# Performance work log

Hardware: AMD Instinct MI355X
Metric: run time of the kernel (lower is better)

The kernel has to match this reference:

```python
import jax, jax.numpy as jnp
import numpy as np

B = 256          # graphs per batch
NPG = 512        # nodes per data graph
NG = B * NPG     # 131072 data-graph nodes
EG = NG * 8      # 1048576 data-graph edges
NQPG = 16        # nodes per query graph
NQ = B * NQPG    # 4096 query nodes
EQ = NQ * 8      # 32768 query edges
IN, H, L, OUT = 64, 128, 2, 1


def setup_inputs() -> dict:
    key = jax.random.key(0)
    ks = jax.random.split(key, 24)
    # edges constrained within each graph (offset + local index)
    g_off = jnp.repeat(jnp.arange(B, dtype=jnp.int32) * NPG, EG // B)
    q_off = jnp.repeat(jnp.arange(B, dtype=jnp.int32) * NQPG, EQ // B)
    inp = {
        "X": jax.random.normal(ks[0], (NG, IN), jnp.float32),
        "X_q": jax.random.normal(ks[1], (NQ, IN), jnp.float32),
        "g_src": g_off + jax.random.randint(ks[2], (EG,), 0, NPG, jnp.int32),
        "g_dst": g_off + jax.random.randint(ks[3], (EG,), 0, NPG, jnp.int32),
        "g_n2g": jnp.repeat(jnp.arange(B, dtype=jnp.int32), NPG),
        "q_src": q_off + jax.random.randint(ks[4], (EQ,), 0, NQPG, jnp.int32),
        "q_dst": q_off + jax.random.randint(ks[5], (EQ,), 0, NQPG, jnp.int32),
        "q_n2g": jnp.repeat(jnp.arange(B, dtype=jnp.int32), NQPG),
    }
    def lin(k, fi, fo):
        s = 1.0 / np.sqrt(fi)
        return jax.random.uniform(k, (fi, fo), jnp.float32, -s, s)
    inp["Wg"] = lin(ks[6], IN, H); inp["bg"] = jnp.zeros((H,), jnp.float32)
    inp["Wq"] = lin(ks[7], IN, H); inp["bq"] = jnp.zeros((H,), jnp.float32)
    inp["betas_g"] = jnp.ones((L,), jnp.float32)  # AGNN beta, init 1
    inp["betas_q"] = jnp.ones((L,), jnp.float32)
    inp["W1r"] = jnp.stack([lin(jax.random.fold_in(ks[8], l), 2 * H, H) for l in range(L)])
    inp["b1r"] = jnp.zeros((L, H), jnp.float32)
    inp["W2r"] = jnp.stack([lin(jax.random.fold_in(ks[9], l), H, H) for l in range(L)])
    inp["b2r"] = jnp.zeros((L, H), jnp.float32)
    inp["Wp1"] = lin(ks[10], H, H); inp["bp1"] = jnp.zeros((H,), jnp.float32)
    inp["Wp2"] = lin(ks[11], H, OUT); inp["bp2"] = jnp.zeros((OUT,), jnp.float32)
    return inp


def agnn(h, src, dst, beta, n):
    # DGL AGNNConv: edge logit = beta * cos(h_dst, h_src); softmax over in-edges of dst;
    # output_i = sum_j alpha_ij * h_j. Nodes with no in-edges get zeros.
    hn = h * jax.lax.rsqrt(jnp.sum(h * h, -1, keepdims=True) + 1e-24)
    e = beta * jnp.sum(hn[src] * hn[dst], -1)                      # [E]
    m = jax.ops.segment_max(e, dst, num_segments=n)
    m = jnp.where(jnp.isfinite(m), m, 0.0)
    ee = jnp.exp(e - m[dst])
    den = jax.ops.segment_sum(ee, dst, num_segments=n)             # [N]
    num = jax.ops.segment_sum(ee[:, None] * h[src], dst, num_segments=n)
    return jnp.where(den[:, None] > 0, num / jnp.maximum(den, 1e-24)[:, None], 0.0)


def reference(X, X_q, g_src, g_dst, g_n2g, q_src, q_dst, q_n2g,
              Wg, bg, Wq, bq, betas_g, betas_q, W1r, b1r, W2r, b2r,
              Wp1, bp1, Wp2, bp2):
    h_g = X @ Wg + bg              # [NG, H]
    h_q = X_q @ Wq + bq            # [NQ, H]
    for l in range(L):
        h_q = agnn(h_q, q_src, q_dst, betas_q[l], NQ)
        h_q_aggr = jax.ops.segment_sum(h_q, q_n2g, num_segments=B)        # dgl.sum_nodes -> [B, H]
        h_cat = jnp.concatenate([h_g, h_q_aggr[g_n2g]], axis=-1)          # per-node broadcast, [NG, 2H]
        h = agnn(h_cat, g_src, g_dst, betas_g[l], NG)                     # [NG, 2H]
        h_g = jax.nn.relu(h @ W1r[l] + b1r[l]) @ W2r[l] + b2r[l]          # MLP reduce -> [NG, H]
    hg_sum = jax.ops.segment_sum(h_g, g_n2g, num_segments=B)             # sum-pool per graph
    y = jax.nn.relu(hg_sum @ Wp1 + bp1) @ Wp2 + bp2                       # SumPredictor -> [B, OUT]
    return y
```

## Files before the change

kernel.cpp:

```cpp
#include <hip/hip_runtime.h>
#include <stdint.h>

#define B_   256
#define NPG  512
#define NG   131072
#define EPG  4096
#define NQPG 16
#define NQ   4096
#define EQPG 128
#define L_   2
#define HPITCH 136

typedef __attribute__((ext_vector_type(8))) short short8;
typedef __attribute__((ext_vector_type(4))) float floatx4;
typedef __attribute__((ext_vector_type(2))) float float2v;

__device__ inline float bf2f(unsigned short u){
    union { unsigned int i; float f; } x; x.i = ((unsigned int)u) << 16; return x.f;
}
__device__ inline unsigned short f2bf(float f){
    union { float f; unsigned int i; } x; x.f = f;
    unsigned int r = x.i + 0x7fff + ((x.i >> 16) & 1);
    return (unsigned short)(r >> 16);
}
__device__ inline float2v bf2x2(unsigned int u){
    union { unsigned int i; float f; } lo, hi;
    lo.i = u << 16; hi.i = u & 0xffff0000u;
    float2v r; r.x = lo.f; r.y = hi.f; return r;
}
__device__ inline float d2(unsigned int a, unsigned int b, float c){
#if __has_builtin(__builtin_amdgcn_fdot2_f32_bf16)
    typedef __attribute__((ext_vector_type(2))) __bf16 bf16x2;
    union { unsigned int u; bf16x2 v; } xa, xb;
    xa.u = a; xb.u = b;
    return __builtin_amdgcn_fdot2_f32_bf16(xa.v, xb.v, c, false);
#else
    union { unsigned int u; float f; } la, ha, lb, hb;
    la.u = a << 16; ha.u = a & 0xffff0000u;
    lb.u = b << 16; hb.u = b & 0xffff0000u;
    return fmaf(la.f, lb.f, fmaf(ha.f, hb.f, c));
#endif
}
__device__ inline float dot8(uint4 a, uint4 b){
    return d2(a.x,b.x, d2(a.y,b.y, d2(a.z,b.z, d2(a.w,b.w, 0.f))));
}
__device__ inline float dot8q(uint4 a, uint4 b, float c0){
    return d2(a.x,b.x, d2(a.y,b.y, d2(a.z,b.z, d2(a.w,b.w, c0))));
}

#if __has_builtin(__builtin_amdgcn_exp2f)
#define FEXP2(x) __builtin_amdgcn_exp2f(x)
#else
#define FEXP2(x) __expf((x) * 0.6931471805599453f)
#endif
#define LOG2E_ 1.4426950408889634f

__device__ inline float red16dpp(float v){
#if __has_builtin(__builtin_amdgcn_mov_dpp)
    int i;
    i = __builtin_amdgcn_mov_dpp(__float_as_int(v), 0xB1, 0xF, 0xF, true);
    v += __int_as_float(i);
    i = __builtin_amdgcn_mov_dpp(__float_as_int(v), 0x4E, 0xF, 0xF, true);
    v += __int_as_float(i);
    i = __builtin_amdgcn_mov_dpp(__float_as_int(v), 0x141, 0xF, 0xF, true);
    v += __int_as_float(i);
    i = __builtin_amdgcn_mov_dpp(__float_as_int(v), 0x128, 0xF, 0xF, true);
    v += __int_as_float(i);
    return v;
#else
    v += __shfl_xor(v,1); v += __shfl_xor(v,2);
    v += __shfl_xor(v,4); v += __shfl_xor(v,8);
    return v;
#endif
}

__device__ inline void red16dpp4(float& v0, float& v1, float& v2, float& v3){
#if defined(__gfx950__) || defined(__gfx942__) || defined(__gfx90a__)
    asm volatile(
        "s_nop 1\n\t"
        "v_add_f32_dpp %0, %0, %0 quad_perm:[1,0,3,2] row_mask:0xf bank_mask:0xf\n\t"
        "v_add_f32_dpp %1, %1, %1 quad_perm:[1,0,3,2] row_mask:0xf bank_mask:0xf\n\t"
        "v_add_f32_dpp %2, %2, %2 quad_perm:[1,0,3,2] row_mask:0xf bank_mask:0xf\n\t"
        "v_add_f32_dpp %3, %3, %3 quad_perm:[1,0,3,2] row_mask:0xf bank_mask:0xf\n\t"
        "v_add_f32_dpp %0, %0, %0 quad_perm:[2,3,0,1] row_mask:0xf bank_mask:0xf\n\t"
        "v_add_f32_dpp %1, %1, %1 quad_perm:[2,3,0,1] row_mask:0xf bank_mask:0xf\n\t"
        "v_add_f32_dpp %2, %2, %2 quad_perm:[2,3,0,1] row_mask:0xf bank_mask:0xf\n\t"
        "v_add_f32_dpp %3, %3, %3 quad_perm:[2,3,0,1] row_mask:0xf bank_mask:0xf\n\t"
        "v_add_f32_dpp %0, %0, %0 row_half_mirror row_mask:0xf bank_mask:0xf\n\t"
        "v_add_f32_dpp %1, %1, %1 row_half_mirror row_mask:0xf bank_mask:0xf\n\t"
        "v_add_f32_dpp %2, %2, %2 row_half_mirror row_mask:0xf bank_mask:0xf\n\t"
        "v_add_f32_dpp %3, %3, %3 row_half_mirror row_mask:0xf bank_mask:0xf\n\t"
        "v_add_f32_dpp %0, %0, %0 row_ror:8 row_mask:0xf bank_mask:0xf\n\t"
        "v_add_f32_dpp %1, %1, %1 row_ror:8 row_mask:0xf bank_mask:0xf\n\t"
        "v_add_f32_dpp %2, %2, %2 row_ror:8 row_mask:0xf bank_mask:0xf\n\t"
        "v_add_f32_dpp %3, %3, %3 row_ror:8 row_mask:0xf bank_mask:0xf"
        : "+v"(v0), "+v"(v1), "+v"(v2), "+v"(v3));
#else
    v0 = red16dpp(v0); v1 = red16dpp(v1); v2 = red16dpp(v2); v3 = red16dpp(v3);
#endif
}

#define ACCUM8(p0,p1,p2,p3,p4,p5,p6,p7,e,u) do { \
    p0 = fmaf(e, bf2f((unsigned short)((u).x&0xffffu)), p0); \
    p1 = fmaf(e, bf2f((unsigned short)((u).x>>16)),    p1); \
    p2 = fmaf(e, bf2f((unsigned short)((u).y&0xffffu)), p2); \
    p3 = fmaf(e, bf2f((unsigned short)((u).y>>16)),    p3); \
    p4 = fmaf(e, bf2f((unsigned short)((u).z&0xffffu)), p4); \
    p5 = fmaf(e, bf2f((unsigned short)((u).z>>16)),    p5); \
    p6 = fmaf(e, bf2f((unsigned short)((u).w&0xffffu)), p6); \
    p7 = fmaf(e, bf2f((unsigned short)((u).w>>16)),    p7); \
} while(0)

#define SMEM_MEGA 11008
__global__ __launch_bounds__(256) void k_mega(
        const int* __restrict__ g_src, const int* __restrict__ g_dst,
        const float* __restrict__ Wg, const float* __restrict__ W1r,
        const float* __restrict__ W2r,
        unsigned short* __restrict__ WgT, unsigned short* __restrict__ W1aT,
        unsigned short* __restrict__ W2rT,
        unsigned short* __restrict__ csrc_g, int* __restrict__ off_g,
        float* __restrict__ degf, unsigned short* __restrict__ nodeperm,
        const float* __restrict__ X_q,
        const float* __restrict__ Wq, const float* __restrict__ bq,
        const int* __restrict__ q_src, const int* __restrict__ q_dst,
        const float* __restrict__ betas_q,
        float* __restrict__ Qv, float* __restrict__ cg2a,
        const float* __restrict__ X,
        const unsigned short* __restrict__ WgT_in,
        const float* __restrict__ bg,
        unsigned short* __restrict__ h_g, float* __restrict__ nrm2){
    extern __shared__ __align__(16) char smem[];
    int bid = blockIdx.x, t = threadIdx.x;
    if (bid < B_){
        int g = bid, lane = t & 63;
        int* cnt   = (int*)smem;
        int* woff  = (int*)(smem + 2048);
        int* gscan = (int*)(smem + 4096);
        int* dh    = (int*)(smem + 4352);
        int* dhoff = (int*)(smem + 4608);
        for (int idx = g*256 + t; idx < 73728; idx += 65536){
            if (idx < 8192){
                int k = idx >> 7, n = idx & 127; WgT[n*64 + k] = f2bf(Wg[idx]);
            } else if (idx < 40960){
                int i = idx - 8192; int l = i >> 14; int j = i & 16383;
                int k = j>>7, n = j&127;
                W1aT[l*16384 + n*128 + k] = f2bf(W1r[l*32768 + j]);
            } else {
                int i = idx - 40960; int l = i >> 14; int j = i & 16383;
                int k = j>>7, n = j&127;
                W2rT[l*16384 + n*128 + k] = f2bf(W2r[i]);
            }
        }
        int gbase = g*NPG; size_t ebase = (size_t)g*EPG;
        for (int n=t;n<NPG;n+=256) cnt[n]=0;
        if (t<64) dh[t]=0;
        __syncthreads();
        for (int i=t;i<EPG;i+=256){
            int d = g_dst[ebase+i]-gbase;
            atomicAdd(&cnt[d],1);
        }
        __syncthreads();
        if (t < 64){
            int s=0;
            #pragma unroll
            for (int j=0;j<8;j++) s += cnt[t*8+j];
            int v=s;
            #pragma unroll
            for (int o=1;o<64;o<<=1){ int u=__shfl_up(v,o); if (lane>=o) v+=u; }
            gscan[t]=v;
        }
        __syncthreads();
        for (int n=t;n<NPG;n+=256){
            int grp=n>>3; int base = grp?gscan[grp-1]:0;
            for (int j=grp*8;j<n;j++) base+=cnt[j];
            off_g[g*NPG+n]=base; woff[n]=base;
            degf[gbase+n] = cnt[n]>0 ? 1.f : 0.f;
            atomicAdd(&dh[cnt[n] < 63 ? cnt[n] : 63], 1);
        }
        __syncthreads();
        if (t < 64){
            int v = dh[t];
            #pragma unroll
            for (int o=1;o<64;o<<=1){ int u=__shfl_up(v,o); if (lane>=o) v+=u; }
            dhoff[t] = v - dh[t];
        }
        __syncthreads();
        for (int n=t;n<NPG;n+=256){
            int d = cnt[n] < 63 ? cnt[n] : 63;
            int pos = atomicAdd(&dhoff[d],1);
            nodeperm[g*NPG+pos] = (unsigned short)n;
        }
        __syncthreads();
        for (int i=t;i<EPG;i+=256){
            int s = g_src[ebase+i]-gbase;
            int d = g_dst[ebase+i]-gbase;
            int pos = atomicAdd(&woff[d],1);
            csrc_g[ebase+pos]=(unsigned short)s;
        }
    } else if (bid < 2*B_){
        int g = bid - B_, sl = t & 15;
        unsigned short* hqrows = (unsigned short*)smem;
        float* xq              = (float*)(smem + 4352);
        float* eq              = (float*)(smem + 8448);
        unsigned short* srcq   = (unsigned short*)(smem + 8960);
        unsigned short* dstq   = (unsigned short*)(smem + 9216);
        float* invq            = (float*)(smem + 9472);
        float* denq            = (float*)(smem + 9536);
        float* hqa             = (float*)(smem + 9600);
        float* cg2s            = (float*)(smem + 10112);
        unsigned int* emaskw   = (unsigned int*)(smem + 10624);
        float* QaccL           = (float*)(smem + 10880);
        for (int i=t;i<NQPG*64;i+=256) xq[i] = X_q[(size_t)g*NQPG*64 + i];
        if (t < EQPG){
            srcq[t] = (unsigned short)(q_src[(size_t)g*EQPG+t] - g*NQPG);
            dstq[t] = (unsigned short)(q_dst[(size_t)g*EQPG+t] - g*NQPG);
        }
        __syncthreads();
        {
            int r = t >> 4, c0 = sl*8;
            float v[8];
            #pragma unroll
            for (int j=0;j<8;j++) v[j] = bq[c0+j];
            for (int k=0;k<64;k++){
                float x = xq[r*64+k];
                const float* wr = Wq + k*128 + c0;
                #pragma unroll
                for (int j=0;j<8;j++) v[j] = fmaf(x, wr[j], v[j]);
            }
            uint4 uu;
            uu.x = (unsigned int)f2bf(v[0]) | ((unsigned int)f2bf(v[1])<<16);
            uu.y = (unsigned int)f2bf(v[2]) | ((unsigned int)f2bf(v[3])<<16);
            uu.z = (unsigned int)f2bf(v[4]) | ((unsigned int)f2bf(v[5])<<16);
            uu.w = (unsigned int)f2bf(v[6]) | ((unsigned int)f2bf(v[7])<<16);
            *(uint4*)(hqrows + r*HPITCH + sl*8) = uu;
        }
        int qn = t >> 4;
        for (int l=0; l<L_; l++){
            float beta_q = betas_q[l];
            if (t < NQPG) denq[t] = 0.f;
            if (t == 16) QaccL[0] = 0.f;
            if (t >= 32 && t < 96) emaskw[t-32] = 0u;
            if (t >= 128 && t < 256) cg2s[t-128] = 0.f;
            __syncthreads();
            {
                uint4 u = *(const uint4*)(hqrows + qn*HPITCH + sl*8);
                float s = red16dpp(dot8(u,u));
                if (sl==0) invq[qn] = rsqrtf(s + 1e-24f);
            }
            __syncthreads();
            for (int e = qn; e < EQPG; e += 16){
                int s = srcq[e], d = dstq[e];
                uint4 us = *(const uint4*)(hqrows + s*HPITCH + sl*8);
                uint4 ud = *(const uint4*)(hqrows + d*HPITCH + sl*8);
                float v = red16dpp(dot8(us, ud));
                if (sl==0){
                    float ee = __expf(beta_q * v * invq[s] * invq[d]);
                    eq[e] = ee;
                    atomicAdd(&denq[d], ee);
                    atomicOr(&emaskw[d*4 + (e>>5)], 1u << (e & 31));
                }
            }
            __syncthreads();
            uint4 nq; nq.x=0; nq.y=0; nq.z=0; nq.w=0;
            {
                float wsum = denq[qn];
                if (wsum > 0.f){
                    float a0=0,a1=0,a2=0,a3=0,a4=0,a5=0,a6=0,a7=0;
                    #pragma unroll
                    for (int w=0;w<4;w++){
                        unsigned int m = emaskw[qn*4+w];
                        while (m){
                            int b = __ffs(m)-1; m &= m-1;
                            int e = w*32 + b;
                            float wg = eq[e];
                            int s = srcq[e];
                            uint4 u = *(const uint4*)(hqrows + s*HPITCH + sl*8);
                            ACCUM8(a0,a1,a2,a3,a4,a5,a6,a7, wg, u);
                        }
                    }
                    float iw = __frcp_rn(wsum);
                    nq.x = (unsigned int)f2bf(a0*iw) | ((unsigned int)f2bf(a1*iw)<<16);
                    nq.y = (unsigned int)f2bf(a2*iw) | ((unsigned int)f2bf(a3*iw)<<16);
                    nq.z = (unsigned int)f2bf(a4*iw) | ((unsigned int)f2bf(a5*iw)<<16);
                    nq.w = (unsigned int)f2bf(a6*iw) | ((unsigned int)f2bf(a7*iw)<<16);
                }
            }
            __syncthreads();
            *(uint4*)(hqrows + qn*HPITCH + sl*8) = nq;
            __syncthreads();
            if (t < 128){
                float s = 0.f;
                for (int n=0;n<NQPG;n++) s += bf2f(hqrows[n*HPITCH + t]);
                hqa[t] = s;
                float qs = s*s;
                #pragma unroll
                for (int o=1;o<64;o<<=1) qs += __shfl_xor(qs, o);
                if ((t & 63) == 0) atomicAdd(&QaccL[0], qs);
            }
            __syncthreads();
            if (t == 0) Qv[l*B_+g] = QaccL[0];
            {
                int jj = t & 127, kc = t >> 7;
                const float* Wl = W1r + (size_t)l*32768;
                float p = 0.f;
                for (int k = kc*64; k < kc*64+64; k++)
                    p = fmaf(hqa[k], Wl[(size_t)(128+k)*128 + jj], p);
                atomicAdd(&cg2s[jj], p);
            }
            __syncthreads();
            if (t < 128) cg2a[((size_t)l*B_+g)*128 + t] = cg2s[t];
            __syncthreads();
        }
    } else {
        const int K = 64;
        int blk = bid - 2*B_;
        int wave = t >> 6, lane = t & 63;
        int quad = lane >> 4, l16 = lane & 15;
        int wrow = blk*64 + wave*16;
        floatx4 acc[8];
        #pragma unroll
        for (int t8=0;t8<8;t8++){
            #pragma unroll
            for (int r=0;r<4;r++) acc[t8][r]=0.f;
        }
        #pragma unroll
        for (int ks = 0; ks < 2; ks++){
            int koff = ks*32 + quad*8;
            const float* ap = X + (size_t)(wrow+l16)*K + koff;
            short8 a;
            #pragma unroll
            for (int j=0;j<8;j++) a[j] = (short)f2bf(ap[j]);
            #pragma unroll
            for (int t8=0;t8<8;t8++){
                short8 b = *(const short8*)(WgT_in + (size_t)(t8*16+l16)*K + koff);
                acc[t8] = __builtin_amdgcn_mfma_f32_16x16x32_bf16(a, b, acc[t8], 0,0,0);
            }
        }
        float ss[4] = {0.f,0.f,0.f,0.f};
        #pragma unroll
        for (int t8=0;t8<8;t8++){
            int col = t8*16 + l16;
            float bv = bg[col];
            #pragma unroll
            for (int r=0;r<4;r++){
                float v = acc[t8][r] + bv;
                h_g[(size_t)(wrow + quad*4 + r)*128 + col] = f2bf(v);
                ss[r] += v*v;
            }
        }
        #pragma unroll
        for (int r=0;r<4;r++){
            #pragma unroll
            for (int o=1;o<16;o<<=1) ss[r] += __shfl_xor(ss[r], o);
        }
        if (l16==0){
            #pragma unroll
            for (int r=0;r<4;r++) nrm2[wrow + quad*4 + r] = ss[r];
        }
    }
}

#define SMEM_GS 152592
#define CIDX(x) ((x) < je1 ? (x) : je1)
#define ROW(i) (*(const uint4*)(hrows + (i)*HPITCH + sl*8))
#define COMP4(U0,U1,U2,U3,I0,I1,I2,I3,JB) do { \
    float v0 = dot8q(U0, ud, Qs); \
    float v1 = dot8q(U1, ud, Qs); \
    float v2 = dot8q(U2, ud, Qs); \
    float v3 = dot8q(U3, ud, Qs); \
    red16dpp4(v0, v1, v2, v3); \
    float e0 = FEXP2(v0 * I0 * bn); \
    float e1 = FEXP2(v1 * I1 * bn); \
    float e2 = FEXP2(v2 * I2 * bn); \
    float e3 = FEXP2(v3 * I3 * bn); \
    if ((JB)+1 >= jend) e1 = 0.f; \
    if ((JB)+2 >= jend) e2 = 0.f; \
    if ((JB)+3 >= jend) e3 = 0.f; \
    ws += (e0 + e1) + (e2 + e3); \
    ax += e0 * bf2x2(U0.x); ay += e0 * bf2x2(U0.y); \
    az += e0 * bf2x2(U0.z); aw += e0 * bf2x2(U0.w); \
    ax += e1 * bf2x2(U1.x); ay += e1 * bf2x2(U1.y); \
    az += e1 * bf2x2(U1.z); aw += e1 * bf2x2(U1.w); \
    ax += e2 * bf2x2(U2.x); ay += e2 * bf2x2(U2.y); \
    az += e2 * bf2x2(U2.z); aw += e2 * bf2x2(U2.w); \
    ax += e3 * bf2x2(U3.x); ay += e3 * bf2x2(U3.y); \
    az += e3 * bf2x2(U3.z); aw += e3 * bf2x2(U3.w); \
} while(0)
__global__ __launch_bounds__(1024) void k_gstage(
        const unsigned short* __restrict__ h_g,
        const float* __restrict__ nrm2,
        const float* __restrict__ betag_p,
        const float* __restrict__ Qv_l,
        const unsigned short* __restrict__ csrc_g,
        const int* __restrict__ off_g,
        const unsigned short* __restrict__ nodeperm,
        unsigned short* __restrict__ aout){
    extern __shared__ __align__(16) char smem[];
    unsigned short* hrows = (unsigned short*)smem;
    float* inv            = (float*)(smem + 139264);
    unsigned short* ssrc  = (unsigned short*)(smem + 141312);
    int* offc             = (int*)(smem + 149504);
    unsigned short* nprm  = (unsigned short*)(smem + 151556);
    int g = blockIdx.x, t = threadIdx.x;
    int group = t >> 4, sl = t & 15;
    float beta_g = betag_p[0];
    int gbase = g*NPG;
    size_t ebase = (size_t)g*EPG;
    float Q = Qv_l[g];
    for (int i=t; i<8192; i+=1024){
        int row = i >> 4, col = i & 15;
        *(uint4*)(hrows + row*HPITCH + col*8) =
            *(const uint4*)(h_g + (size_t)(gbase+row)*128 + col*8);
    }
    for (int n=t; n<NPG; n+=1024){
        inv[n] = rsqrtf(nrm2[gbase+n] + Q + 1e-24f);
        nprm[n] = nodeperm[g*NPG+n];
    }
    for (int i=t; i<EPG; i+=1024) ssrc[i] = csrc_g[ebase+i];
    for (int n=t; n<=NPG; n+=1024) offc[n] = (n<NPG) ? off_g[g*NPG+n] : EPG;
    __syncthreads();
    float Qs = Q * 0.0625f;
    for (int idx = group; idx < NPG; idx += 64){
        int n = nprm[idx];
        int o = offc[n];
        int jend = offc[n+1];
        uint4 ov;
        if (jend > o){
            uint4 ud = *(const uint4*)(hrows + n*HPITCH + sl*8);
            float bn = beta_g * inv[n] * LOG2E_;
            float ws = 0.f;
            float2v ax; ax.x=0.f; ax.y=0.f;
            float2v ay = ax, az = ax, aw = ax;
            int je1 = jend - 1;
            int iA0 = ssrc[o];
            int iA1 = ssrc[CIDX(o+1)];
            int iA2 = ssrc[CIDX(o+2)];
            int iA3 = ssrc[CIDX(o+3)];
            uint4 uA0 = ROW(iA0);
            uint4 uA1 = ROW(iA1);
            uint4 uA2 = ROW(iA2);
            uint4 uA3 = ROW(iA3);
            float vA0 = inv[iA0], vA1 = inv[iA1], vA2 = inv[iA2], vA3 = inv[iA3];
            int iB0 = ssrc[CIDX(o+4)];
            int iB1 = ssrc[CIDX(o+5)];
            int iB2 = ssrc[CIDX(o+6)];
            int iB3 = ssrc[CIDX(o+7)];
            int j = o;
            for (;;){
                uint4 uB0 = ROW(iB0);
                uint4 uB1 = ROW(iB1);
                uint4 uB2 = ROW(iB2);
                uint4 uB3 = ROW(iB3);
                float vB0 = inv[iB0], vB1 = inv[iB1], vB2 = inv[iB2], vB3 = inv[iB3];
                iA0 = ssrc[CIDX(j+8)];
                iA1 = ssrc[CIDX(j+9)];
                iA2 = ssrc[CIDX(j+10)];
                iA3 = ssrc[CIDX(j+11)];
                COMP4(uA0,uA1,uA2,uA3, vA0,vA1,vA2,vA3, j);
                j += 4; if (j >= jend) break;
                uA0 = ROW(iA0);
                uA1 = ROW(iA1);
                uA2 = ROW(iA2);
                uA3 = ROW(iA3);
                vA0 = inv[iA0]; vA1 = inv[iA1]; vA2 = inv[iA2]; vA3 = inv[iA3];
                iB0 = ssrc[CIDX(j+8)];
                iB1 = ssrc[CIDX(j+9)];
                iB2 = ssrc[CIDX(j+10)];
                iB3 = ssrc[CIDX(j+11)];
                COMP4(uB0,uB1,uB2,uB3, vB0,vB1,vB2,vB3, j);
                j += 4; if (j >= jend) break;
            }
            float iw = __frcp_rn(ws);
            ov.x = (unsigned int)f2bf(ax.x*iw) | ((unsigned int)f2bf(ax.y*iw)<<16);
            ov.y = (unsigned int)f2bf(ay.x*iw) | ((unsigned int)f2bf(ay.y*iw)<<16);
            ov.z = (unsigned int)f2bf(az.x*iw) | ((unsigned int)f2bf(az.y*iw)<<16);
            ov.w = (unsigned int)f2bf(aw.x*iw) | ((unsigned int)f2bf(aw.y*iw)<<16);
        } else {
            ov.x=0; ov.y=0; ov.z=0; ov.w=0;
        }
        *(uint4*)(aout + (size_t)(gbase+n)*128 + sl*8) = ov;
    }
}

#define SMEM_MLP (3*128*136*2 + 1024)
__global__ __launch_bounds__(512, 2) void k_mlp_p(const unsigned short* __restrict__ A,
        const unsigned short* __restrict__ W1t, const float* __restrict__ b1,
        const float* __restrict__ cg2, const float* __restrict__ degf,
        const unsigned short* __restrict__ W2t, const float* __restrict__ b2,
        unsigned short* __restrict__ out, float* __restrict__ nrm2out,
        const float* __restrict__ Wp1, const float* __restrict__ bp1,
        const float* __restrict__ Wp2, const float* __restrict__ bp2,
        float* __restrict__ y){
    extern __shared__ __align__(16) char smem[];
    unsigned short* W1s = (unsigned short*)smem;
    unsigned short* W2s = W1s + 128*136;
    unsigned short* h1  = W2s + 128*136;
    float* hsum = (float*)(smem + 3*128*136*2);
    float* red2 = hsum + 128;
    int t = threadIdx.x;
    int g = blockIdx.x;
    #pragma unroll
    for (int p=0;p<4;p++){
        int flat = p*4096 + t*8;
        int n = flat>>7, k = flat&127;
        *(uint4*)(W1s + n*136 + k) = *(const uint4*)(W1t + n*128 + k);
        *(uint4*)(W2s + n*136 + k) = *(const uint4*)(W2t + n*128 + k);
    }
    if (y && t < 128) hsum[t] = 0.f;
    __syncthreads();
    int wave = t>>6, lane = t&63, quad = lane>>4, l16 = lane&15;
    const float* cg = cg2 + (size_t)g*128;
    float psum[8];
    #pragma unroll
    for (int j=0;j<8;j++) psum[j] = 0.f;
    short8 af[4];
    {
        int wrow = g*512 + wave*16;
        #pragma unroll
        for (int ks=0;ks<4;ks++)
            af[ks] = *(const short8*)(A + (size_t)(wrow+l16)*128 + ks*32 + quad*8);
    }
    for (int it=0; it<4; it++){
        int wrow = g*512 + it*128 + wave*16;
        floatx4 acc[8];
        #pragma unroll
        for (int t8=0;t8<8;t8++){
            #pragma unroll
            for (int r=0;r<4;r++) acc[t8][r]=0.f;
        }
        #pragma unroll
        for (int ks=0;ks<4;ks++){
            int koff = ks*32 + quad*8;
            #pragma unroll
            for (int t8=0;t8<8;t8++){
                short8 b = *(const short8*)(W1s + (t8*16+l16)*136 + koff);
                acc[t8] = __builtin_amdgcn_mfma_f32_16x16x32_bf16(af[ks], b, acc[t8], 0,0,0);
            }
        }
        float dg[4];
        #pragma unroll
        for (int r=0;r<4;r++) dg[r] = degf[wrow + quad*4 + r];
        #pragma unroll
        for (int t8=0;t8<8;t8++){
            int col = t8*16 + l16;
            float bv = b1[col];
            float cv = cg[col];
            #pragma unroll
            for (int r=0;r<4;r++){
                float v = acc[t8][r] + bv + dg[r]*cv;
                v = v > 0.f ? v : 0.f;
                h1[(wave*16 + quad*4 + r)*136 + col] = f2bf(v);
            }
        }
        __syncthreads();
        short8 afn[4];
        if (it < 3){
            int wrow_n = g*512 + (it+1)*128 + wave*16;
            #pragma unroll
            for (int ks=0;ks<4;ks++)
                afn[ks] = *(const short8*)(A + (size_t)(wrow_n+l16)*128 + ks*32 + quad*8);
        }
        short8 hf[4];
        #pragma unroll
        for (int ks=0;ks<4;ks++) hf[ks] = *(const short8*)(h1 + (wave*16+l16)*136 + ks*32 + quad*8);
        floatx4 acc2[8];
        #pragma unroll
        for (int t8=0;t8<8;t8++){
            #pragma unroll
            for (int r=0;r<4;r++) acc2[t8][r]=0.f;
        }
        #pragma unroll
        for (int ks=0;ks<4;ks++){
            int koff = ks*32 + quad*8;
            #pragma unroll
            for (int t8=0;t8<8;t8++){
                short8 b = *(const short8*)(W2s + (t8*16+l16)*136 + koff);
                acc2[t8] = __builtin_amdgcn_mfma_f32_16x16x32_bf16(hf[ks], b, acc2[t8], 0,0,0);
            }
        }
        float ss[4] = {0.f,0.f,0.f,0.f};
        #pragma unroll
        for (int t8=0;t8<8;t8++){
            int col = t8*16 + l16;
            float bv = b2[col];
            #pragma unroll
            for (int r=0;r<4;r++){
                float v = acc2[t8][r] + bv;
                if (y){
                    psum[t8] += v;
                } else {
                    out[(size_t)(wrow + quad*4 + r)*128 + col] = f2bf(v);
                }
                ss[r] += v*v;
            }
        }
        if (nrm2out){
            #pragma unroll
            for (int r=0;r<4;r++){
                #pragma unroll
                for (int o=1;o<16;o<<=1) ss[r] += __shfl_xor(ss[r], o);
            }
            if (l16==0){
                #pragma unroll
                for (int r=0;r<4;r++)
                    nrm2out[wrow + quad*4 + r] = ss[r];
            }
        }
        __syncthreads();
        #pragma unroll
        for (int ks=0;ks<4;ks++) af[ks] = afn[ks];
    }
    if (y){
        #pragma unroll
        for (int j=0;j<8;j++){
            psum[j] += __shfl_xor(psum[j], 16);
            psum[j] += __shfl_xor(psum[j], 32);
        }
        if (lane < 16){
            #pragma unroll
            for (int j=0;j<8;j++) atomicAdd(&hsum[j*16 + lane], psum[j]);
        }
        __syncthreads();
        if (t < 128){
            float acc = bp1[t];
            for (int k=0;k<128;k++) acc += hsum[k]*Wp1[k*128+t];
            acc = fmaxf(acc, 0.f);
            red2[t] = acc * Wp2[t];
        }
        __syncthreads();
        for (int s2=64; s2>0; s2>>=1){
            if (t<s2) red2[t]+=red2[t+s2];
            __syncthreads();
        }
        if (t==0) y[g] = red2[0] + bp2[0];
    }
}

extern "C" void kernel_launch(void* const* d_in, const int* in_sizes, int n_in,
                              void* d_out, int out_size, void* d_ws, size_t ws_size,
                              hipStream_t stream) {
    const float* X    = (const float*)d_in[0];
    const float* X_q  = (const float*)d_in[1];
    const int* g_src = (const int*)d_in[2];
    const int* g_dst = (const int*)d_in[3];
    const int* q_src = (const int*)d_in[5];
    const int* q_dst = (const int*)d_in[6];
    const float* Wg   = (const float*)d_in[8];
    const float* bg   = (const float*)d_in[9];
    const float* Wq   = (const float*)d_in[10];
    const float* bq   = (const float*)d_in[11];
    const float* betas_g = (const float*)d_in[12];
    const float* betas_q = (const float*)d_in[13];
    const float* W1r  = (const float*)d_in[14];
    const float* b1r  = (const float*)d_in[15];
    const float* W2r  = (const float*)d_in[16];
    const float* b2r  = (const float*)d_in[17];
    const float* Wp1  = (const float*)d_in[18];
    const float* bp1  = (const float*)d_in[19];
    const float* Wp2  = (const float*)d_in[20];
    const float* bp2  = (const float*)d_in[21];

    uint8_t* w = (uint8_t*)d_ws;
    unsigned short* h_g  = (unsigned short*)w;    w += (size_t)NG*128*2;
    unsigned short* aout = (unsigned short*)w;    w += (size_t)NG*128*2;
    float* nrm2  = (float*)w;                     w += (size_t)NG*4;
    float* degf  = (float*)w;                     w += (size_t)NG*4;
    float* Qv    = (float*)w;                     w += (size_t)L_*B_*4;
    float* cg2a  = (float*)w;                     w += (size_t)L_*B_*128*4;
    unsigned short* WgT   = (unsigned short*)w;   w += 8192*2;
    unsigned short* W1aT  = (unsigned short*)w;   w += 2*16384*2;
    unsigned short* W2rT  = (unsigned short*)w;   w += 2*16384*2;
    unsigned short* csrc_g = (unsigned short*)w;  w += (size_t)B_*EPG*2;
    unsigned short* nodeperm = (unsigned short*)w; w += (size_t)B_*NPG*2;
    int* off_g = (int*)w;                         w += (size_t)B_*NPG*4;

    static bool attr_done = false;
    if (!attr_done){
        hipFuncSetAttribute((const void*)k_mlp_p,
                            hipFuncAttributeMaxDynamicSharedMemorySize, SMEM_MLP);
        hipFuncSetAttribute((const void*)k_gstage,
                            hipFuncAttributeMaxDynamicSharedMemorySize, SMEM_GS);
        attr_done = true;
    }

    k_mega<<<2*B_ + NG/64, 256, SMEM_MEGA, stream>>>(
        g_src, g_dst, Wg, W1r, W2r, WgT, W1aT, W2rT,
        csrc_g, off_g, degf, nodeperm,
        X_q, Wq, bq, q_src, q_dst, betas_q, Qv, cg2a,
        X, WgT, bg, h_g, nrm2);
    for (int l=0;l<L_;l++){
        k_gstage<<<B_,1024,SMEM_GS,stream>>>(h_g, nrm2, betas_g + l, Qv + l*B_,
                                             csrc_g, off_g, nodeperm, aout);
        k_mlp_p<<<B_,512,SMEM_MLP,stream>>>(aout, W1aT + l*16384, b1r + l*128,
                                            cg2a + (size_t)l*B_*128, degf,
                                            W2rT + l*16384, b2r + l*128, h_g,
                                            (l==0) ? nrm2 : nullptr,
                                            Wp1, bp1, Wp2, bp2,
                                            (l==L_-1) ? (float*)d_out : nullptr);
    }
}
```

Measured before the change: 260.7 us.

## Fuse both layers of graph attention and MLP into one per-graph kernel

Replaces the four per-layer launches (attention stage plus MLP per layer) with a single kernel, one block per graph, that loops over both layers. The updated node features stay in shared memory instead of round-tripping through global memory. The MLP now runs on only 2 of the 16 waves, in 16 serialized passes. It reads weights directly from global memory instead of staging them in shared memory, and derives the degree indicator from the CSR offsets. This removes launch overhead and the h_g write/read between stages, at the cost of poor MFMA parallelism in the MLP phase and one resident 1024-thread block per CU.

```diff
diff --git a/kernel.cpp b/kernel.cpp
--- a/kernel.cpp
+++ b/kernel.cpp
@@ -360,7 +360,7 @@
     }
 }
 
-#define SMEM_GS 152592
+#define SMEM_UBER 162320
 #define CIDX(x) ((x) < je1 ? (x) : je1)
 #define ROW(i) (*(const uint4*)(hrows + (i)*HPITCH + sl*8))
 #define COMP4(U0,U1,U2,U3,I0,I1,I2,I3,JB) do { \
@@ -386,231 +386,217 @@
     ax += e3 * bf2x2(U3.x); ay += e3 * bf2x2(U3.y); \
     az += e3 * bf2x2(U3.z); aw += e3 * bf2x2(U3.w); \
 } while(0)
-__global__ __launch_bounds__(1024) void k_gstage(
+__global__ __launch_bounds__(1024) void k_uber(
         const unsigned short* __restrict__ h_g,
-        const float* __restrict__ nrm2,
-        const float* __restrict__ betag_p,
-        const float* __restrict__ Qv_l,
+        const float* __restrict__ nrm2g,
+        const float* __restrict__ betas_g,
+        const float* __restrict__ Qv,
         const unsigned short* __restrict__ csrc_g,
         const int* __restrict__ off_g,
         const unsigned short* __restrict__ nodeperm,
-        unsigned short* __restrict__ aout){
+        const unsigned short* __restrict__ W1aT, const float* __restrict__ b1r,
+        const float* __restrict__ cg2a,
+        const unsigned short* __restrict__ W2rT, const float* __restrict__ b2r,
+        const float* __restrict__ Wp1, const float* __restrict__ bp1,
+        const float* __restrict__ Wp2, const float* __restrict__ bp2,
+        unsigned short* __restrict__ aout, float* __restrict__ y){
     extern __shared__ __align__(16) char smem[];
     unsigned short* hrows = (unsigned short*)smem;
     float* inv            = (float*)(smem + 139264);
     unsigned short* ssrc  = (unsigned short*)(smem + 141312);
     int* offc             = (int*)(smem + 149504);
     unsigned short* nprm  = (unsigned short*)(smem + 151556);
+    unsigned short* h1    = (unsigned short*)(smem + 152592);
+    float* hsum           = (float*)(smem + 161296);
+    float* red2           = (float*)(smem + 161808);
     int g = blockIdx.x, t = threadIdx.x;
     int group = t >> 4, sl = t & 15;
-    float beta_g = betag_p[0];
     int gbase = g*NPG;
     size_t ebase = (size_t)g*EPG;
-    float Q = Qv_l[g];
+    int wave = t>>6, lane = t&63, quad = lane>>4, l16 = lane&15;
     for (int i=t; i<8192; i+=1024){
         int row = i >> 4, col = i & 15;
         *(uint4*)(hrows + row*HPITCH + col*8) =
             *(const uint4*)(h_g + (size_t)(gbase+row)*128 + col*8);
     }
     for (int n=t; n<NPG; n+=1024){
-        inv[n] = rsqrtf(nrm2[gbase+n] + Q + 1e-24f);
+        inv[n] = nrm2g[gbase+n];
         nprm[n] = nodeperm[g*NPG+n];
     }
     for (int i=t; i<EPG; i+=1024) ssrc[i] = csrc_g[ebase+i];
     for (int n=t; n<=NPG; n+=1024) offc[n] = (n<NPG) ? off_g[g*NPG+n] : EPG;
-    __syncthreads();
-    float Qs = Q * 0.0625f;
-    for (int idx = group; idx < NPG; idx += 64){
-        int n = nprm[idx];
-        int o = offc[n];
-        int jend = offc[n+1];
-        uint4 ov;
-        if (jend > o){
-            uint4 ud = *(const uint4*)(hrows + n*HPITCH + sl*8);
-            float bn = beta_g * inv[n] * LOG2E_;
-            float ws = 0.f;
-            float2v ax; ax.x=0.f; ax.y=0.f;
-            float2v ay = ax, az = ax, aw = ax;
-            int je1 = jend - 1;
-            int iA0 = ssrc[o];
-            int iA1 = ssrc[CIDX(o+1)];
-            int iA2 = ssrc[CIDX(o+2)];
-            int iA3 = ssrc[CIDX(o+3)];
-            uint4 uA0 = ROW(iA0);
-            uint4 uA1 = ROW(iA1);
-            uint4 uA2 = ROW(iA2);
-            uint4 uA3 = ROW(iA3);
-            float vA0 = inv[iA0], vA1 = inv[iA1], vA2 = inv[iA2], vA3 = inv[iA3];
-            int iB0 = ssrc[CIDX(o+4)];
-            int iB1 = ssrc[CIDX(o+5)];
-            int iB2 = ssrc[CIDX(o+6)];
-            int iB3 = ssrc[CIDX(o+7)];
-            int j = o;
-            for (;;){
-                uint4 uB0 = ROW(iB0);
-                uint4 uB1 = ROW(iB1);
-                uint4 uB2 = ROW(iB2);
-                uint4 uB3 = ROW(iB3);
-                float vB0 = inv[iB0], vB1 = inv[iB1], vB2 = inv[iB2], vB3 = inv[iB3];
-                iA0 = ssrc[CIDX(j+8)];
-                iA1 = ssrc[CIDX(j+9)];
-                iA2 = ssrc[CIDX(j+10)];
-                iA3 = ssrc[CIDX(j+11)];
-                COMP4(uA0,uA1,uA2,uA3, vA0,vA1,vA2,vA3, j);
-                j += 4; if (j >= jend) break;
-                uA0 = ROW(iA0);
-                uA1 = ROW(iA1);
-                uA2 = ROW(iA2);
-                uA3 = ROW(iA3);
-                vA0 = inv[iA0]; vA1 = inv[iA1]; vA2 = inv[iA2]; vA3 = inv[iA3];
-                iB0 = ssrc[CIDX(j+8)];
-                iB1 = ssrc[CIDX(j+9)];
-                iB2 = ssrc[CIDX(j+10)];
-                iB3 = ssrc[CIDX(j+11)];
-                COMP4(uB0,uB1,uB2,uB3, vB0,vB1,vB2,vB3, j);
-                j += 4; if (j >= jend) break;
-            }
-            float iw = __frcp_rn(ws);
-            ov.x = (unsigned int)f2bf(ax.x*iw) | ((unsigned int)f2bf(ax.y*iw)<<16);
-            ov.y = (unsigned int)f2bf(ay.x*iw) | ((unsigned int)f2bf(ay.y*iw)<<16);
-            ov.z = (unsigned int)f2bf(az.x*iw) | ((unsigned int)f2bf(az.y*iw)<<16);
-            ov.w = (unsigned int)f2bf(aw.x*iw) | ((unsigned int)f2bf(aw.y*iw)<<16);
-        } else {
-            ov.x=0; ov.y=0; ov.z=0; ov.w=0;
-        }
-        *(uint4*)(aout + (size_t)(gbase+n)*128 + sl*8) = ov;
-    }
-}
-
-#define SMEM_MLP (3*128*136*2 + 1024)
-__global__ __launch_bounds__(512, 2) void k_mlp_p(const unsigned short* __restrict__ A,
-        const unsigned short* __restrict__ W1t, const float* __restrict__ b1,
-        const float* __restrict__ cg2, const float* __restrict__ degf,
-        const unsigned short* __restrict__ W2t, const float* __restrict__ b2,
-        unsigned short* __restrict__ out, float* __restrict__ nrm2out,
-        const float* __restrict__ Wp1, const float* __restrict__ bp1,
-        const float* __restrict__ Wp2, const float* __restrict__ bp2,
-        float* __restrict__ y){
-    extern __shared__ __align__(16) char smem[];
-    unsigned short* W1s = (unsigned short*)smem;
-    unsigned short* W2s = W1s + 128*136;
-    unsigned short* h1  = W2s + 128*136;
-    float* hsum = (float*)(smem + 3*128*136*2);
-    float* red2 = hsum + 128;
-    int t = threadIdx.x;
-    int g = blockIdx.x;
-    #pragma unroll
-    for (int p=0;p<4;p++){
-        int flat = p*4096 + t*8;
-        int n = flat>>7, k = flat&127;
-        *(uint4*)(W1s + n*136 + k) = *(const uint4*)(W1t + n*128 + k);
-        *(uint4*)(W2s + n*136 + k) = *(const uint4*)(W2t + n*128 + k);
-    }
-    if (y && t < 128) hsum[t] = 0.f;
-    __syncthreads();
-    int wave = t>>6, lane = t&63, quad = lane>>4, l16 = lane&15;
-    const float* cg = cg2 + (size_t)g*128;
+    if (t < 128) hsum[t] = 0.f;
     float psum[8];
     #pragma unroll
     for (int j=0;j<8;j++) psum[j] = 0.f;
-    short8 af[4];
-    {
-        int wrow = g*512 + wave*16;
-        #pragma unroll
-        for (int ks=0;ks<4;ks++)
-            af[ks] = *(const short8*)(A + (size_t)(wrow+l16)*128 + ks*32 + quad*8);
-    }
-    for (int it=0; it<4; it++){
-        int wrow = g*512 + it*128 + wave*16;
-        floatx4 acc[8];
-        #pragma unroll
-        for (int t8=0;t8<8;t8++){
-            #pragma unroll
-            for (int r=0;r<4;r++) acc[t8][r]=0.f;
-        }
-        #pragma unroll
-        for (int ks=0;ks<4;ks++){
-            int koff = ks*32 + quad*8;
-            #pragma unroll
-            for (int t8=0;t8<8;t8++){
-                short8 b = *(const short8*)(W1s + (t8*16+l16)*136 + koff);
-                acc[t8] = __builtin_amdgcn_mfma_f32_16x16x32_bf16(af[ks], b, acc[t8], 0,0,0);
-            }
-        }
-        float dg[4];
-        #pragma unroll
-        for (int r=0;r<4;r++) dg[r] = degf[wrow + quad*4 + r];
-        #pragma unroll
-        for (int t8=0;t8<8;t8++){
-            int col = t8*16 + l16;
-            float bv = b1[col];
-            float cv = cg[col];
-            #pragma unroll
-            for (int r=0;r<4;r++){
-                float v = acc[t8][r] + bv + dg[r]*cv;
-                v = v > 0.f ? v : 0.f;
-                h1[(wave*16 + quad*4 + r)*136 + col] = f2bf(v);
-            }
-        }
-        __syncthreads();
-        short8 afn[4];
-        if (it < 3){
-            int wrow_n = g*512 + (it+1)*128 + wave*16;
-            #pragma unroll
-            for (int ks=0;ks<4;ks++)
-                afn[ks] = *(const short8*)(A + (size_t)(wrow_n+l16)*128 + ks*32 + quad*8);
-        }
-        short8 hf[4];
-        #pragma unroll
-        for (int ks=0;ks<4;ks++) hf[ks] = *(const short8*)(h1 + (wave*16+l16)*136 + ks*32 + quad*8);
-        floatx4 acc2[8];
-        #pragma unroll
-        for (int t8=0;t8<8;t8++){
-            #pragma unroll
-            for (int r=0;r<4;r++) acc2[t8][r]=0.f;
-        }
-        #pragma unroll
-        for (int ks=0;ks<4;ks++){
-            int koff = ks*32 + quad*8;
-            #pragma unroll
-            for (int t8=0;t8<8;t8++){
-                short8 b = *(const short8*)(W2s + (t8*16+l16)*136 + koff);
-                acc2[t8] = __builtin_amdgcn_mfma_f32_16x16x32_bf16(hf[ks], b, acc2[t8], 0,0,0);
-            }
-        }
-        float ss[4] = {0.f,0.f,0.f,0.f};
-        #pragma unroll
-        for (int t8=0;t8<8;t8++){
-            int col = t8*16 + l16;
-            float bv = b2[col];
-            #pragma unroll
-            for (int r=0;r<4;r++){
-                float v = acc2[t8][r] + bv;
-                if (y){
-                    psum[t8] += v;
-                } else {
-                    out[(size_t)(wrow + quad*4 + r)*128 + col] = f2bf(v);
-                }
-                ss[r] += v*v;
-            }
-        }
-        if (nrm2out){
-            #pragma unroll
-            for (int r=0;r<4;r++){
-                #pragma unroll
-                for (int o=1;o<16;o<<=1) ss[r] += __shfl_xor(ss[r], o);
-            }
-            if (l16==0){
-                #pragma unroll
-                for (int r=0;r<4;r++)
-                    nrm2out[wrow + quad*4 + r] = ss[r];
-            }
-        }
-        __syncthreads();
-        #pragma unroll
-        for (int ks=0;ks<4;ks++) af[ks] = afn[ks];
-    }
-    if (y){
+    __syncthreads();
+    for (int l=0; l<L_; l++){
+        float Q = Qv[l*B_+g];
+        float beta_g = betas_g[l];
+        unsigned short* aoutl = aout + (size_t)l*NG*128;
+        for (int n=t;n<NPG;n+=1024) inv[n] = rsqrtf(inv[n] + Q + 1e-24f);
+        __syncthreads();
+        float Qs = Q * 0.0625f;
+        for (int idx = group; idx < NPG; idx += 64){
+            int n = nprm[idx];
+            int o = offc[n];
+            int jend = offc[n+1];
+            uint4 ov;
+            if (jend > o){
+                uint4 ud = *(const uint4*)(hrows + n*HPITCH + sl*8);
+                float bn = beta_g * inv[n] * LOG2E_;
+                float ws = 0.f;
+                float2v ax; ax.x=0.f; ax.y=0.f;
+                float2v ay = ax, az = ax, aw = ax;
+                int je1 = jend - 1;
+                int iA0 = ssrc[o];
+                int iA1 = ssrc[CIDX(o+1)];
+                int iA2 = ssrc[CIDX(o+2)];
+                int iA3 = ssrc[CIDX(o+3)];
+                uint4 uA0 = ROW(iA0);
+                uint4 uA1 = ROW(iA1);
+                uint4 uA2 = ROW(iA2);
+                uint4 uA3 = ROW(iA3);
+                float vA0 = inv[iA0], vA1 = inv[iA1], vA2 = inv[iA2], vA3 = inv[iA3];
+                int iB0 = ssrc[CIDX(o+4)];
+                int iB1 = ssrc[CIDX(o+5)];
+                int iB2 = ssrc[CIDX(o+6)];
+                int iB3 = ssrc[CIDX(o+7)];
+                int j = o;
+                for (;;){
+                    uint4 uB0 = ROW(iB0);
+                    uint4 uB1 = ROW(iB1);
+                    uint4 uB2 = ROW(iB2);
+                    uint4 uB3 = ROW(iB3);
+                    float vB0 = inv[iB0], vB1 = inv[iB1], vB2 = inv[iB2], vB3 = inv[iB3];
+                    iA0 = ssrc[CIDX(j+8)];
+                    iA1 = ssrc[CIDX(j+9)];
+                    iA2 = ssrc[CIDX(j+10)];
+                    iA3 = ssrc[CIDX(j+11)];
+                    COMP4(uA0,uA1,uA2,uA3, vA0,vA1,vA2,vA3, j);
+                    j += 4; if (j >= jend) break;
+                    uA0 = ROW(iA0);
+                    uA1 = ROW(iA1);
+                    uA2 = ROW(iA2);
+                    uA3 = ROW(iA3);
+                    vA0 = inv[iA0]; vA1 = inv[iA1]; vA2 = inv[iA2]; vA3 = inv[iA3];
+                    iB0 = ssrc[CIDX(j+8)];
+                    iB1 = ssrc[CIDX(j+9)];
+                    iB2 = ssrc[CIDX(j+10)];
+                    iB3 = ssrc[CIDX(j+11)];
+                    COMP4(uB0,uB1,uB2,uB3, vB0,vB1,vB2,vB3, j);
+                    j += 4; if (j >= jend) break;
+                }
+                float iw = __frcp_rn(ws);
+                ov.x = (unsigned int)f2bf(ax.x*iw) | ((unsigned int)f2bf(ax.y*iw)<<16);
+                ov.y = (unsigned int)f2bf(ay.x*iw) | ((unsigned int)f2bf(ay.y*iw)<<16);
+                ov.z = (unsigned int)f2bf(az.x*iw) | ((unsigned int)f2bf(az.y*iw)<<16);
+                ov.w = (unsigned int)f2bf(aw.x*iw) | ((unsigned int)f2bf(aw.y*iw)<<16);
+            } else {
+                ov.x=0; ov.y=0; ov.z=0; ov.w=0;
+            }
+            *(uint4*)(aoutl + (size_t)(gbase+n)*128 + sl*8) = ov;
+        }
+        __syncthreads();
+        const unsigned short* W1t = W1aT + l*16384;
+        const unsigned short* W2t = W2rT + l*16384;
+        const float* b1 = b1r + l*128;
+        const float* b2 = b2r + l*128;
+        const float* cg = cg2a + ((size_t)l*B_ + g)*128;
+        const int last = (l == L_-1);
+        for (int pass=0; pass<16; pass++){
+            if (wave < 2){
+                int rowb = pass*32 + wave*16;
+                short8 af[4];
+                #pragma unroll
+                for (int ks=0;ks<4;ks++)
+                    af[ks] = *(const short8*)(aoutl +
+                        (size_t)(gbase+rowb+l16)*128 + ks*32 + quad*8);
+                floatx4 acc[8];
+                #pragma unroll
+                for (int t8=0;t8<8;t8++){
+                    #pragma unroll
+                    for (int r=0;r<4;r++) acc[t8][r]=0.f;
+                }
+                #pragma unroll
+                for (int ks=0;ks<4;ks++){
+                    int koff = ks*32 + quad*8;
+                    #pragma unroll
+                    for (int t8=0;t8<8;t8++){
+                        short8 b = *(const short8*)(W1t + (size_t)(t8*16+l16)*128 + koff);
+                        acc[t8] = __builtin_amdgcn_mfma_f32_16x16x32_bf16(af[ks], b, acc[t8], 0,0,0);
+                    }
+                }
+                #pragma unroll
+                for (int t8=0;t8<8;t8++){
+                    int col = t8*16 + l16;
+                    float bv = b1[col];
+                    float cv = cg[col];
+                    #pragma unroll
+                    for (int r=0;r<4;r++){
+                        int row = rowb + quad*4 + r;
+                        float dgv = (offc[row+1] > offc[row]) ? 1.f : 0.f;
+                        float v = acc[t8][r] + bv + dgv*cv;
+                        v = v > 0.f ? v : 0.f;
+                        h1[(wave*16 + quad*4 + r)*136 + col] = f2bf(v);
+                    }
+                }
+            }
+            __syncthreads();
+            if (wave < 2){
+                int rowb = pass*32 + wave*16;
+                short8 hf[4];
+                #pragma unroll
+                for (int ks=0;ks<4;ks++)
+                    hf[ks] = *(const short8*)(h1 + (wave*16+l16)*136 + ks*32 + quad*8);
+                floatx4 acc2[8];
+                #pragma unroll
+                for (int t8=0;t8<8;t8++){
+                    #pragma unroll
+                    for (int r=0;r<4;r++) acc2[t8][r]=0.f;
+                }
+                #pragma unroll
+                for (int ks=0;ks<4;ks++){
+                    int koff = ks*32 + quad*8;
+                    #pragma unroll
+                    for (int t8=0;t8<8;t8++){
+                        short8 b = *(const short8*)(W2t + (size_t)(t8*16+l16)*128 + koff);
+                        acc2[t8] = __builtin_amdgcn_mfma_f32_16x16x32_bf16(hf[ks], b, acc2[t8], 0,0,0);
+                    }
+                }
+                float ss[4] = {0.f,0.f,0.f,0.f};
+                #pragma unroll
+                for (int t8=0;t8<8;t8++){
+                    int col = t8*16 + l16;
+                    float bv = b2[col];
+                    #pragma unroll
+                    for (int r=0;r<4;r++){
+                        float v = acc2[t8][r] + bv;
+                        if (last){
+                            psum[t8] += v;
+                        } else {
+                            hrows[(rowb + quad*4 + r)*HPITCH + col] = f2bf(v);
+                            ss[r] += v*v;
+                        }
+                    }
+                }
+                if (!last){
+                    #pragma unroll
+                    for (int r=0;r<4;r++){
+                        #pragma unroll
+                        for (int o=1;o<16;o<<=1) ss[r] += __shfl_xor(ss[r], o);
+                    }
+                    if (l16==0){
+                        #pragma unroll
+                        for (int r=0;r<4;r++)
+                            inv[rowb + quad*4 + r] = ss[r];
+                    }
+                }
+            }
+            __syncthreads();
+        }
+    }
+    if (wave < 2){
         #pragma unroll
         for (int j=0;j<8;j++){
             psum[j] += __shfl_xor(psum[j], 16);
@@ -620,20 +606,20 @@
             #pragma unroll
             for (int j=0;j<8;j++) atomicAdd(&hsum[j*16 + lane], psum[j]);
         }
-        __syncthreads();
-        if (t < 128){
-            float acc = bp1[t];
-            for (int k=0;k<128;k++) acc += hsum[k]*Wp1[k*128+t];
-            acc = fmaxf(acc, 0.f);
-            red2[t] = acc * Wp2[t];
-        }
-        __syncthreads();
-        for (int s2=64; s2>0; s2>>=1){
-            if (t<s2) red2[t]+=red2[t+s2];
-            __syncthreads();
-        }
-        if (t==0) y[g] = red2[0] + bp2[0];
-    }
+    }
+    __syncthreads();
+    if (t < 128){
+        float acc = bp1[t];
+        for (int k=0;k<128;k++) acc += hsum[k]*Wp1[k*128+t];
+        acc = fmaxf(acc, 0.f);
+        red2[t] = acc * Wp2[t];
+    }
+    __syncthreads();
+    for (int s2=64; s2>0; s2>>=1){
+        if (t<s2) red2[t]+=red2[t+s2];
+        __syncthreads();
+    }
+    if (t==0) y[g] = red2[0] + bp2[0];
 }
 
 extern "C" void kernel_launch(void* const* d_in, const int* in_sizes, int n_in,
@@ -662,7 +648,7 @@
 
     uint8_t* w = (uint8_t*)d_ws;
     unsigned short* h_g  = (unsigned short*)w;    w += (size_t)NG*128*2;
-    unsigned short* aout = (unsigned short*)w;    w += (size_t)NG*128*2;
+    unsigned short* aout = (unsigned short*)w;    w += (size_t)L_*NG*128*2;
     float* nrm2  = (float*)w;                     w += (size_t)NG*4;
     float* degf  = (float*)w;                     w += (size_t)NG*4;
     float* Qv    = (float*)w;                     w += (size_t)L_*B_*4;
@@ -676,10 +662,8 @@
 
     static bool attr_done = false;
     if (!attr_done){
-        hipFuncSetAttribute((const void*)k_mlp_p,
-                            hipFuncAttributeMaxDynamicSharedMemorySize, SMEM_MLP);
-        hipFuncSetAttribute((const void*)k_gstage,
-                            hipFuncAttributeMaxDynamicSharedMemorySize, SMEM_GS);
+        hipFuncSetAttribute((const void*)k_uber,
+                            hipFuncAttributeMaxDynamicSharedMemorySize, SMEM_UBER);
         attr_done = true;
     }
 
@@ -688,14 +672,8 @@
         csrc_g, off_g, degf, nodeperm,
         X_q, Wq, bq, q_src, q_dst, betas_q, Qv, cg2a,
         X, WgT, bg, h_g, nrm2);
-    for (int l=0;l<L_;l++){
-        k_gstage<<<B_,1024,SMEM_GS,stream>>>(h_g, nrm2, betas_g + l, Qv + l*B_,
-                                             csrc_g, off_g, nodeperm, aout);
-        k_mlp_p<<<B_,512,SMEM_MLP,stream>>>(aout, W1aT + l*16384, b1r + l*128,
-                                            cg2a + (size_t)l*B_*128, degf,
-                                            W2rT + l*16384, b2r + l*128, h_g,
-                                            (l==0) ? nrm2 : nullptr,
-                                            Wp1, bp1, Wp2, bp2,
-                                            (l==L_-1) ? (float*)d_out : nullptr);
-    }
-}
+    k_uber<<<B_, 1024, SMEM_UBER, stream>>>(
+        h_g, nrm2, betas_g, Qv, csrc_g, off_g, nodeperm,
+        W1aT, b1r, cg2a, W2rT, b2r,
+        Wp1, bp1, Wp2, bp2, aout, (float*)d_out);
+}
```

Result: slower. 624.4 us (+139.5%).

## Fuse graph attention stage and MLP reduce into one per-graph kernel

Applied to the files above, without the earlier changes.

Merges the AGNN aggregation kernel and the two-layer MLP kernel into a single kernel per layer. Each block now handles one graph end to end. After the aggregation it reuses the shared memory for the weight tiles and reads back its own freshly written rows while they are still cache-hot. The degree indicator comes from the shared-memory CSR offsets instead of a separate global array. This drops one launch per layer and the inter-kernel round trip, but the MLP now runs at one 1024-thread block per graph instead of the earlier 512-thread, two-blocks-per-CU configuration.

```diff
diff --git a/kernel.cpp b/kernel.cpp
--- a/kernel.cpp
+++ b/kernel.cpp
@@ -360,7 +360,7 @@
     }
 }
 
-#define SMEM_GS 152592
+#define SMEM_GM 152592
 #define CIDX(x) ((x) < je1 ? (x) : je1)
 #define ROW(i) (*(const uint4*)(hrows + (i)*HPITCH + sl*8))
 #define COMP4(U0,U1,U2,U3,I0,I1,I2,I3,JB) do { \
@@ -386,15 +386,22 @@
     ax += e3 * bf2x2(U3.x); ay += e3 * bf2x2(U3.y); \
     az += e3 * bf2x2(U3.z); aw += e3 * bf2x2(U3.w); \
 } while(0)
-__global__ __launch_bounds__(1024) void k_gstage(
+__global__ __launch_bounds__(1024) void k_gm(
         const unsigned short* __restrict__ h_g,
-        const float* __restrict__ nrm2,
+        const float* __restrict__ nrm2g,
         const float* __restrict__ betag_p,
         const float* __restrict__ Qv_l,
         const unsigned short* __restrict__ csrc_g,
         const int* __restrict__ off_g,
         const unsigned short* __restrict__ nodeperm,
-        unsigned short* __restrict__ aout){
+        unsigned short* __restrict__ aout,
+        const unsigned short* __restrict__ W1t, const float* __restrict__ b1,
+        const float* __restrict__ cg2, const unsigned short* __restrict__ W2t,
+        const float* __restrict__ b2,
+        unsigned short* __restrict__ hg_out, float* __restrict__ nrm2out,
+        const float* __restrict__ Wp1, const float* __restrict__ bp1,
+        const float* __restrict__ Wp2, const float* __restrict__ bp2,
+        float* __restrict__ y){
     extern __shared__ __align__(16) char smem[];
     unsigned short* hrows = (unsigned short*)smem;
     float* inv            = (float*)(smem + 139264);
@@ -406,6 +413,7 @@
     float beta_g = betag_p[0];
     int gbase = g*NPG;
     size_t ebase = (size_t)g*EPG;
+    int wave = t>>6, lane = t&63, quad = lane>>4, l16 = lane&15;
     float Q = Qv_l[g];
     for (int i=t; i<8192; i+=1024){
         int row = i >> 4, col = i & 15;
@@ -413,7 +421,7 @@
             *(const uint4*)(h_g + (size_t)(gbase+row)*128 + col*8);
     }
     for (int n=t; n<NPG; n+=1024){
-        inv[n] = rsqrtf(nrm2[gbase+n] + Q + 1e-24f);
+        inv[n] = rsqrtf(nrm2g[gbase+n] + Q + 1e-24f);
         nprm[n] = nodeperm[g*NPG+n];
     }
     for (int i=t; i<EPG; i+=1024) ssrc[i] = csrc_g[ebase+i];
@@ -480,48 +488,31 @@
         }
         *(uint4*)(aout + (size_t)(gbase+n)*128 + sl*8) = ov;
     }
-}
-
-#define SMEM_MLP (3*128*136*2 + 1024)
-__global__ __launch_bounds__(512, 2) void k_mlp_p(const unsigned short* __restrict__ A,
-        const unsigned short* __restrict__ W1t, const float* __restrict__ b1,
-        const float* __restrict__ cg2, const float* __restrict__ degf,
-        const unsigned short* __restrict__ W2t, const float* __restrict__ b2,
-        unsigned short* __restrict__ out, float* __restrict__ nrm2out,
-        const float* __restrict__ Wp1, const float* __restrict__ bp1,
-        const float* __restrict__ Wp2, const float* __restrict__ bp2,
-        float* __restrict__ y){
-    extern __shared__ __align__(16) char smem[];
+    __syncthreads();
     unsigned short* W1s = (unsigned short*)smem;
     unsigned short* W2s = W1s + 128*136;
     unsigned short* h1  = W2s + 128*136;
-    float* hsum = (float*)(smem + 3*128*136*2);
+    float* hsum = (float*)(smem + 139264);
     float* red2 = hsum + 128;
-    int t = threadIdx.x;
-    int g = blockIdx.x;
     #pragma unroll
-    for (int p=0;p<4;p++){
-        int flat = p*4096 + t*8;
+    for (int p=0;p<2;p++){
+        int flat = p*8192 + t*8;
         int n = flat>>7, k = flat&127;
         *(uint4*)(W1s + n*136 + k) = *(const uint4*)(W1t + n*128 + k);
         *(uint4*)(W2s + n*136 + k) = *(const uint4*)(W2t + n*128 + k);
     }
-    if (y && t < 128) hsum[t] = 0.f;
     __syncthreads();
-    int wave = t>>6, lane = t&63, quad = lane>>4, l16 = lane&15;
+    const int last = (y != nullptr);
     const float* cg = cg2 + (size_t)g*128;
     float psum[8];
     #pragma unroll
     for (int j=0;j<8;j++) psum[j] = 0.f;
-    short8 af[4];
-    {
-        int wrow = g*512 + wave*16;
+    for (int it=0; it<2; it++){
+        int rowb = it*256 + wave*16;
+        short8 af[4];
         #pragma unroll
         for (int ks=0;ks<4;ks++)
-            af[ks] = *(const short8*)(A + (size_t)(wrow+l16)*128 + ks*32 + quad*8);
-    }
-    for (int it=0; it<4; it++){
-        int wrow = g*512 + it*128 + wave*16;
+            af[ks] = *(const short8*)(aout + (size_t)(gbase+rowb+l16)*128 + ks*32 + quad*8);
         floatx4 acc[8];
         #pragma unroll
         for (int t8=0;t8<8;t8++){
@@ -537,9 +528,7 @@
                 acc[t8] = __builtin_amdgcn_mfma_f32_16x16x32_bf16(af[ks], b, acc[t8], 0,0,0);
             }
         }
-        float dg[4];
-        #pragma unroll
-        for (int r=0;r<4;r++) dg[r] = degf[wrow + quad*4 + r];
+        int lrow = wave*16;
         #pragma unroll
         for (int t8=0;t8<8;t8++){
             int col = t8*16 + l16;
@@ -547,22 +536,18 @@
             float cv = cg[col];
             #pragma unroll
             for (int r=0;r<4;r++){
-                float v = acc[t8][r] + bv + dg[r]*cv;
+                int row = rowb + quad*4 + r;
+                float dgv = (offc[row+1] > offc[row]) ? 1.f : 0.f;
+                float v = acc[t8][r] + bv + dgv*cv;
                 v = v > 0.f ? v : 0.f;
-                h1[(wave*16 + quad*4 + r)*136 + col] = f2bf(v);
-            }
-        }
-        __syncthreads();
-        short8 afn[4];
-        if (it < 3){
-            int wrow_n = g*512 + (it+1)*128 + wave*16;
-            #pragma unroll
-            for (int ks=0;ks<4;ks++)
-                afn[ks] = *(const short8*)(A + (size_t)(wrow_n+l16)*128 + ks*32 + quad*8);
-        }
+                h1[(lrow + quad*4 + r)*136 + col] = f2bf(v);
+            }
+        }
+        __syncthreads();
         short8 hf[4];
         #pragma unroll
-        for (int ks=0;ks<4;ks++) hf[ks] = *(const short8*)(h1 + (wave*16+l16)*136 + ks*32 + quad*8);
+        for (int ks=0;ks<4;ks++)
+            hf[ks] = *(const short8*)(h1 + (lrow+l16)*136 + ks*32 + quad*8);
         floatx4 acc2[8];
         #pragma unroll
         for (int t8=0;t8<8;t8++){
@@ -586,15 +571,15 @@
             #pragma unroll
             for (int r=0;r<4;r++){
                 float v = acc2[t8][r] + bv;
-                if (y){
+                if (last){
                     psum[t8] += v;
                 } else {
-                    out[(size_t)(wrow + quad*4 + r)*128 + col] = f2bf(v);
+                    hg_out[(size_t)(gbase + rowb + quad*4 + r)*128 + col] = f2bf(v);
+                    ss[r] += v*v;
                 }
-                ss[r] += v*v;
-            }
-        }
-        if (nrm2out){
+            }
+        }
+        if (!last){
             #pragma unroll
             for (int r=0;r<4;r++){
                 #pragma unroll
@@ -603,14 +588,14 @@
             if (l16==0){
                 #pragma unroll
                 for (int r=0;r<4;r++)
-                    nrm2out[wrow + quad*4 + r] = ss[r];
-            }
-        }
-        __syncthreads();
-        #pragma unroll
-        for (int ks=0;ks<4;ks++) af[ks] = afn[ks];
-    }
-    if (y){
+                    nrm2out[gbase + rowb + quad*4 + r] = ss[r];
+            }
+        }
+        __syncthreads();
+    }
+    if (last){
+        if (t < 128) hsum[t] = 0.f;
+        __syncthreads();
         #pragma unroll
         for (int j=0;j<8;j++){
             psum[j] += __shfl_xor(psum[j], 16);
@@ -676,10 +661,8 @@
 
     static bool attr_done = false;
     if (!attr_done){
-        hipFuncSetAttribute((const void*)k_mlp_p,
-                            hipFuncAttributeMaxDynamicSharedMemorySize, SMEM_MLP);
-        hipFuncSetAttribute((const void*)k_gstage,
-                            hipFuncAttributeMaxDynamicSharedMemorySize, SMEM_GS);
+        hipFuncSetAttribute((const void*)k_gm,
+                            hipFuncAttributeMaxDynamicSharedMemorySize, SMEM_GM);
         attr_done = true;
     }
 
@@ -689,13 +672,13 @@
         X_q, Wq, bq, q_src, q_dst, betas_q, Qv, cg2a,
         X, WgT, bg, h_g, nrm2);
     for (int l=0;l<L_;l++){
-        k_gstage<<<B_,1024,SMEM_GS,stream>>>(h_g, nrm2, betas_g + l, Qv + l*B_,
-                                             csrc_g, off_g, nodeperm, aout);
-        k_mlp_p<<<B_,512,SMEM_MLP,stream>>>(aout, W1aT + l*16384, b1r + l*128,
-                                            cg2a + (size_t)l*B_*128, degf,
-                                            W2rT + l*16384, b2r + l*128, h_g,
-                                            (l==0) ? nrm2 : nullptr,
-                                            Wp1, bp1, Wp2, bp2,
-                                            (l==L_-1) ? (float*)d_out : nullptr);
-    }
-}
+        k_gm<<<B_, 1024, SMEM_GM, stream>>>(
+            h_g, nrm2, betas_g + l, Qv + l*B_,
+            csrc_g, off_g, nodeperm, aout,
+            W1aT + l*16384, b1r + l*128, cg2a + (size_t)l*B_*128,
+            W2rT + l*16384, b2r + l*128,
+            h_g, (l==0) ? nrm2 : nullptr,
+            Wp1, bp1, Wp2, bp2,
+            (l==L_-1) ? (float*)d_out : nullptr);
+    }
+}
```

New measurement: 259.0 us (median of 3 runs). About the same (-0.6%).
